# Optimization experiments

Hardware: AMD Instinct MI355X
Metric: run time of the kernel (lower is better)

## Reference

```python
import jax, jax.numpy as jnp
import numpy as np

K = 3  # kernel_size
KK = K * K


def conv2d(x, w, b, stride=1, padding=1, dilation=1):
    out = jax.lax.conv_general_dilated(
        x, w, (stride, stride), [(padding, padding), (padding, padding)],
        rhs_dilation=(dilation, dilation),
        dimension_numbers=('NCHW', 'OIHW', 'NCHW'))
    return out + b[None, :, None, None]


def bilinear_gather(x, py, px):
    # x: [B,C,H,W]; py,px: [B,KK,H,W] float sampling coords (zero outside).
    B, C, H, W = x.shape
    y0 = jnp.floor(py)
    x0 = jnp.floor(px)
    wy1 = py - y0
    wx1 = px - x0
    xf = x.reshape(B, C, H * W)

    def corner(yc, xc, wgt):
        valid = (yc >= 0) & (yc <= H - 1) & (xc >= 0) & (xc <= W - 1)
        yi = jnp.clip(yc, 0, H - 1).astype(jnp.int32)
        xi = jnp.clip(xc, 0, W - 1).astype(jnp.int32)
        idx = (yi * W + xi).reshape(B, 1, -1)  # [B,1,KK*H*W]
        v = jnp.take_along_axis(xf, jnp.broadcast_to(idx, (B, C, idx.shape[-1])), axis=2)
        v = v.reshape(B, C, *yc.shape[1:])  # [B,C,KK,H,W]
        return v * (wgt * valid)[:, None]

    return (corner(y0, x0, (1 - wy1) * (1 - wx1)) +
            corner(y0, x0 + 1, (1 - wy1) * wx1) +
            corner(y0 + 1, x0, wy1 * (1 - wx1)) +
            corner(y0 + 1, x0 + 1, wy1 * wx1))


def modulated_deform_conv(x, offset, mask, w, b, stride=1, padding=1, dilation=1):
    B, C, H, W = x.shape
    Ho, Wo = offset.shape[2], offset.shape[3]
    off = offset.reshape(B, KK, 2, Ho, Wo)
    dy, dx = off[:, :, 0], off[:, :, 1]  # [B,KK,Ho,Wo]
    ki, kj = jnp.meshgrid(jnp.arange(K), jnp.arange(K), indexing='ij')
    ki = ki.reshape(-1).astype(x.dtype)  # [KK]
    kj = kj.reshape(-1).astype(x.dtype)
    base_y = (jnp.arange(Ho) * stride - padding).astype(x.dtype)
    base_x = (jnp.arange(Wo) * stride - padding).astype(x.dtype)
    py = base_y[None, None, :, None] + (ki * dilation)[None, :, None, None] + dy
    px = base_x[None, None, None, :] + (kj * dilation)[None, :, None, None] + dx
    x_off = bilinear_gather(x, py, px)              # [B,C,KK,Ho,Wo]
    x_off = x_off * mask[:, None]                   # modulation
    w_flat = w.reshape(w.shape[0], C, KK)           # [O,C,KK]
    out = jnp.einsum('bckhw,ock->bohw', x_off, w_flat)
    return out + b[None, :, None, None]


def setup_inputs() -> dict:
    key = jax.random.key(0)
    ks = jax.random.split(key, 7)
    B, C, O, H, W = 8, 64, 64, 128, 128
    x = jax.random.normal(ks[0], (B, C, H, W), dtype=jnp.float32)
    # offset/mask predictor convs (zero-init in the module; randomized small here
    # so offsets/masks are non-trivial for kernel correctness testing)
    p_w = jax.random.normal(ks[1], (2 * KK, C, 3, 3), dtype=jnp.float32) * 0.02
    p_b = jax.random.normal(ks[2], (2 * KK,), dtype=jnp.float32) * 0.1
    m_w = jax.random.normal(ks[3], (KK, C, 3, 3), dtype=jnp.float32) * 0.02
    m_b = jax.random.normal(ks[4], (KK,), dtype=jnp.float32) * 0.1
    # deformable conv weights
    d_w = jax.random.normal(ks[5], (O, C, K, K), dtype=jnp.float32) * (1.0 / np.sqrt(C * KK))
    d_b = jax.random.normal(ks[6], (O,), dtype=jnp.float32) * 0.01
    return {"x": x, "p_w": p_w, "p_b": p_b, "m_w": m_w, "m_b": m_b, "d_w": d_w, "d_b": d_b}


def reference(x, p_w, p_b, m_w, m_b, d_w, d_b):
    offset = conv2d(x, p_w, p_b, stride=1, padding=1, dilation=1)   # [B,18,H,W]
    mask = jax.nn.sigmoid(conv2d(x, m_w, m_b, stride=1, padding=1, dilation=1))  # [B,9,H,W]
    out = modulated_deform_conv(x, offset, mask, d_w, d_b, stride=1, padding=1, dilation=1)
    return (out, offset)
```

## Files before the change

### kernel.cpp

```cpp
#include <hip/hip_runtime.h>
#include <math.h>

#define KK 9
#define BB 8
#define CC 64
#define OO 64
#define HH 128
#define WW 128
#define HWSZ (HH*WW)

typedef _Float16 half8 __attribute__((ext_vector_type(8)));
typedef float    floatx4 __attribute__((ext_vector_type(4)));

#define WP_ELEMS (9*2*4*32*8)
#define WD_ELEMS (9*2*4*64*8)
#define XH_ELEMS ((size_t)BB*HWSZ*64)
#define NCONV 2048

__global__ __launch_bounds__(256) void prep(
    const float* __restrict__ x,
    const float* __restrict__ p_w, const float* __restrict__ m_w,
    const float* __restrict__ d_w,
    _Float16* __restrict__ Wp, _Float16* __restrict__ Wd, _Float16* __restrict__ x_h,
    int conv_blocks)
{
    const int blk = blockIdx.x;
    const int tid = threadIdx.x;
    if (blk < conv_blocks) {
        __shared__ _Float16 sh[64][72];
        const int b    = blk >> 8;
        const int pix0 = (blk & 255) * 64;
        const float* xb = x + (size_t)b*CC*HWSZ + pix0;
        {
            const int p     = tid & 63;
            const int cbase = tid >> 6;
            #pragma unroll
            for (int j = 0; j < 16; ++j) {
                const int c = j*4 + cbase;
                sh[p][c] = (_Float16)xb[(size_t)c*HWSZ + p];
            }
        }
        __syncthreads();
        {
            const int p  = tid >> 2;
            const int c0 = (tid & 3) * 16;
            _Float16* dst = x_h + ((size_t)b*HWSZ + pix0 + p)*64 + c0;
            *(half8*)dst       = *(const half8*)&sh[p][c0];
            *(half8*)(dst + 8) = *(const half8*)&sh[p][c0 + 8];
        }
    } else {
        const int i = (blk - conv_blocks)*256 + tid;
        if (i < WP_ELEMS) {
            const int e = i & 7, n = (i>>3)&31, quad = (i>>8)&3, ks = (i>>10)&1, k = i>>11;
            const int c = ks*32 + quad*8 + e;
            float v = 0.f;
            if (n < 18)      v = p_w[(n*CC + c)*KK + k];
            else if (n < 27) v = m_w[((n-18)*CC + c)*KK + k];
            Wp[i] = (_Float16)v;
        } else if (i < WP_ELEMS + WD_ELEMS) {
            const int j = i - WP_ELEMS;
            const int e = j & 7, o = (j>>3)&63, quad = (j>>9)&3, ks = (j>>11)&1, k = j>>12;
            const int c = ks*32 + quad*8 + e;
            Wd[j] = (_Float16)d_w[(o*CC + c)*KK + k];
        }
    }
}

__global__ __launch_bounds__(256, 3) void dcn_fused(
    const _Float16* __restrict__ x_h,
    const _Float16* __restrict__ Wp, const _Float16* __restrict__ Wd,
    const float* __restrict__ p_b, const float* __restrict__ m_b,
    const float* __restrict__ db,
    float* __restrict__ out, float* __restrict__ offset_out)
{
    __shared__ alignas(16) float    T[27*68];
    __shared__ alignas(16) _Float16 WS[2][4096];

    const int tid  = threadIdx.x;
    const int wv   = tid >> 6;
    const int lane = tid & 63;
    const int quad = lane >> 4;
    const int l15  = lane & 15;
    const int b    = blockIdx.x & 7;
    const int seg  = blockIdx.x >> 3;
    const int row  = seg >> 1;
    const int col0 = (seg & 1) * 64;
    const int pix0 = row * WW + col0;
    const int px   = wv*16 + l15;
    const int wx   = col0 + px;
    const _Float16* xbh = x_h + (size_t)b*HWSZ*64;

    half8 ws0a = *(const half8*)(Wd + tid*16);
    half8 ws0b = *(const half8*)(Wd + tid*16 + 8);

    floatx4 accp[2];
    accp[0] = (floatx4)0.f; accp[1] = (floatx4)0.f;
    #pragma unroll
    for (int k = 0; k < 9; ++k) {
        const int hy = row + k/3 - 1;
        const int hx = wx  + k%3 - 1;
        const bool vld = (hy >= 0) & (hy < HH) & (hx >= 0) & (hx < WW);
        const _Float16* ap = xbh + (size_t)(vld ? hy*WW + hx : 0)*64 + quad*8;
        const half8 z = (half8)(_Float16)0.f;
        half8 a0 = *(const half8*)ap;
        half8 a1 = *(const half8*)(ap + 32);
        a0 = vld ? a0 : z;
        a1 = vld ? a1 : z;
        const _Float16* wp = Wp + k*2048 + quad*256 + l15*8;
        #pragma unroll
        for (int ks = 0; ks < 2; ++ks) {
            const half8 af = ks ? a1 : a0;
            accp[0] = __builtin_amdgcn_mfma_f32_16x16x32_f16(af, *(const half8*)(wp + ks*1024),       accp[0], 0, 0, 0);
            accp[1] = __builtin_amdgcn_mfma_f32_16x16x32_f16(af, *(const half8*)(wp + ks*1024 + 128), accp[1], 0, 0, 0);
        }
    }

    #pragma unroll
    for (int nt = 0; nt < 2; ++nt) {
        const int ch = nt*16 + l15;
        if (ch < 27) {
            const float bias = (ch < 18) ? p_b[ch] : m_b[ch-18];
            #pragma unroll
            for (int r = 0; r < 4; ++r)
                T[ch*68 + wv*16 + quad*4 + r] = accp[nt][r] + bias;
        }
    }
    {
        _Float16* wd = &WS[0][tid*16];
        *(half8*)wd     = ws0a;
        *(half8*)(wd+8) = ws0b;
    }
    __syncthreads();

    {
        float* offp = offset_out + (size_t)b*18*HWSZ + pix0;
        #pragma unroll
        for (int j = 0; j < 5; ++j) {
            const int idx = j*256 + tid;
            if (idx < 18*64) {
                const int ch = idx >> 6, p2i = idx & 63;
                offp[ch*HWSZ + p2i] = T[ch*68 + p2i];
            }
        }
    }

    const int p2   = wv*16 + (lane >> 2);
    const int part = lane & 3;
    const int wx2  = col0 + p2;
    const int bidx = ((l15 << 2) | quad) << 2;

    float dyk[9], dxk[9], mkk[9];
    #pragma unroll
    for (int k = 0; k < 9; ++k) {
        dyk[k] = T[(2*k  )*68 + p2];
        dxk[k] = T[(2*k+1)*68 + p2];
        mkk[k] = 1.f / (1.f + expf(-T[(18+k)*68 + p2]));
    }

    floatx4 acc[4];
    #pragma unroll
    for (int nt = 0; nt < 4; ++nt) acc[nt] = (floatx4)0.f;

    #pragma unroll
    for (int k = 0; k < 9; ++k) {
        half8 wsa, wsb;
        if (k < 8) {
            const _Float16* wsrc = Wd + (k+1)*4096 + tid*16;
            wsa = *(const half8*)wsrc;
            wsb = *(const half8*)(wsrc + 8);
        }

        const float dy = dyk[k], dx = dxk[k], mk = mkk[k];
        const float py  = (float)(row - 1 + k/3) + dy;
        const float pxf = (float)(wx2 - 1 + k%3) + dx;
        const float y0f = floorf(py), x0f = floorf(pxf);
        const int   iy0 = (int)y0f,   ix0 = (int)x0f;
        const float wy1 = py - y0f,   wx1 = pxf - x0f;
        const float wy0 = 1.f - wy1,  wx0 = 1.f - wx1;
        const bool vy0 = ((unsigned)iy0     < (unsigned)HH);
        const bool vy1 = ((unsigned)(iy0+1) < (unsigned)HH);
        const bool vx0 = ((unsigned)ix0     < (unsigned)WW);
        const bool vx1 = ((unsigned)(ix0+1) < (unsigned)WW);
        const int cy0 = min(max(iy0,   0), HH-1), cy1 = min(max(iy0+1, 0), HH-1);
        const int cx0 = min(max(ix0,   0), WW-1), cx1 = min(max(ix0+1, 0), WW-1);
        const int i0 = cy0*WW+cx0, i1 = cy0*WW+cx1, i2 = cy1*WW+cx0, i3 = cy1*WW+cx1;
        const _Float16 g0 = (_Float16)(wy0*wx0*((vy0&vx0) ? mk : 0.f));
        const _Float16 g1 = (_Float16)(wy0*wx1*((vy0&vx1) ? mk : 0.f));
        const _Float16 g2 = (_Float16)(wy1*wx0*((vy1&vx0) ? mk : 0.f));
        const _Float16 g3 = (_Float16)(wy1*wx1*((vy1&vx1) ? mk : 0.f));

        const _Float16* c0p = xbh + (size_t)i0*64 + part*8;
        const _Float16* c1p = xbh + (size_t)i1*64 + part*8;
        const _Float16* c2p = xbh + (size_t)i2*64 + part*8;
        const _Float16* c3p = xbh + (size_t)i3*64 + part*8;
        const half8 p0l = *(const half8*)c0p, p0h = *(const half8*)(c0p + 32);
        const half8 p1l = *(const half8*)c1p, p1h = *(const half8*)(c1p + 32);
        const half8 p2l = *(const half8*)c2p, p2h = *(const half8*)(c2p + 32);
        const half8 p3l = *(const half8*)c3p, p3h = *(const half8*)(c3p + 32);
        const half8 lo = p0l*g0 + p1l*g1 + p2l*g2 + p3l*g3;
        const half8 hi = p0h*g0 + p1h*g1 + p2h*g2 + p3h*g3;

        union U { half8 h; int i[4]; };
        U ulo, uhi, a0u, a1u;
        ulo.h = lo; uhi.h = hi;
        #pragma unroll
        for (int d = 0; d < 4; ++d) {
            a0u.i[d] = __builtin_amdgcn_ds_bpermute(bidx, ulo.i[d]);
            a1u.i[d] = __builtin_amdgcn_ds_bpermute(bidx, uhi.i[d]);
        }

        #pragma unroll
        for (int ks = 0; ks < 2; ++ks) {
            const half8 af = ks ? a1u.h : a0u.h;
            const _Float16* wsp = &WS[k&1][ks*2048 + quad*512 + l15*8];
            #pragma unroll
            for (int nt = 0; nt < 4; ++nt)
                acc[nt] = __builtin_amdgcn_mfma_f32_16x16x32_f16(af, *(const half8*)(wsp + nt*128), acc[nt], 0, 0, 0);
        }

        if (k < 8) {
            _Float16* wd = &WS[(k+1)&1][tid*16];
            *(half8*)wd     = wsa;
            *(half8*)(wd+8) = wsb;
        }
        __syncthreads();
    }

    float* T2 = (float*)&WS[0][0];
    #pragma unroll
    for (int oc = 0; oc < 4; ++oc) {
        #pragma unroll
        for (int r = 0; r < 4; ++r)
            T2[l15*68 + wv*16 + quad*4 + r] = acc[oc][r];
        __syncthreads();
        #pragma unroll
        for (int j = 0; j < 4; ++j) {
            const int idx = j*256 + tid;
            const int o16 = idx >> 6, pp = idx & 63;
            out[((size_t)b*OO + oc*16 + o16)*HWSZ + pix0 + pp] = T2[o16*68 + pp] + db[oc*16 + o16];
        }
        __syncthreads();
    }
}

__global__ __launch_bounds__(256, 4) void dcn_fused_lds(
    const float* __restrict__ x,
    const _Float16* __restrict__ Wp, const _Float16* __restrict__ Wd,
    const float* __restrict__ p_b, const float* __restrict__ m_b,
    const float* __restrict__ db,
    float* __restrict__ out, float* __restrict__ offset_out)
{
    __shared__ alignas(16) _Float16 A_sh[128][72];
    __shared__ alignas(16) _Float16 WM_sh[32*72];
    __shared__ alignas(16) _Float16 Wd_sh[64][72];

    const int tid   = threadIdx.x;
    const int wv    = tid >> 6;
    const int lane  = tid & 63;
    const int quad  = lane >> 4;
    const int l15   = lane & 15;
    const int b     = blockIdx.x & 7;
    const int row   = blockIdx.x >> 3;
    const int pix0  = row * WW;
    const int p     = tid & 127;
    const int chalf = (tid >> 7) * 32;
    const int h = row, w = p;
    const float* xb = x + (size_t)b*CC*HWSZ;
    _Float16 (*W_sh)[72] = (_Float16 (*)[72])WM_sh;

    floatx4 accp[2][2];
    #pragma unroll
    for (int mt = 0; mt < 2; ++mt)
        #pragma unroll
        for (int nt = 0; nt < 2; ++nt) accp[mt][nt] = (floatx4)0.f;

    for (int k = 0; k < 9; ++k) {
        {
            const int n  = tid >> 3;
            const int c0 = (tid & 7) * 8;
            *(half8*)&W_sh[n][c0] =
                *(const half8*)(Wp + k*2048 + (c0>>5)*1024 + ((c0>>3)&3)*256 + n*8);
        }
        const int hy = h + (k/3) - 1;
        const int wx = w + (k%3) - 1;
        const bool vld = (hy >= 0) & (hy < HH) & (wx >= 0) & (wx < WW);
        const float* xs = xb + hy*WW + wx;
        #pragma unroll
        for (int cb = 0; cb < 4; ++cb) {
            union { half8 v; _Float16 e[8]; } u;
            #pragma unroll
            for (int j = 0; j < 8; ++j)
                u.e[j] = (_Float16)(vld ? xs[(size_t)(chalf + cb*8 + j)*HWSZ] : 0.f);
            *(half8*)&A_sh[p][chalf + cb*8] = u.v;
        }
        __syncthreads();
        #pragma unroll
        for (int ks = 0; ks < 2; ++ks) {
            half8 bf[2];
            #pragma unroll
            for (int nt = 0; nt < 2; ++nt)
                bf[nt] = *(const half8*)&W_sh[nt*16 + l15][ks*32 + quad*8];
            #pragma unroll
            for (int mt = 0; mt < 2; ++mt) {
                half8 af = *(const half8*)&A_sh[wv*32 + mt*16 + l15][ks*32 + quad*8];
                accp[mt][0] = __builtin_amdgcn_mfma_f32_16x16x32_f16(af, bf[0], accp[mt][0], 0, 0, 0);
                accp[mt][1] = __builtin_amdgcn_mfma_f32_16x16x32_f16(af, bf[1], accp[mt][1], 0, 0, 0);
            }
        }
        __syncthreads();
    }

    float (*T)[132] = (float (*)[132])&A_sh[0][0];
    #pragma unroll
    for (int nt = 0; nt < 2; ++nt) {
        const int ch = nt*16 + l15;
        if (ch < 27) {
            #pragma unroll
            for (int mt = 0; mt < 2; ++mt)
                #pragma unroll
                for (int r = 0; r < 4; ++r)
                    T[ch][wv*32 + mt*16 + quad*4 + r] = accp[mt][nt][r];
        }
    }
    __syncthreads();

    float dyk[9], dxk[9], mkk[9];
    float* offp = offset_out + (size_t)b*18*HWSZ + pix0;
    #pragma unroll
    for (int k = 0; k < 9; ++k) {
        dyk[k] = T[2*k][p]   + p_b[2*k];
        dxk[k] = T[2*k+1][p] + p_b[2*k+1];
        mkk[k] = 1.f / (1.f + expf(-(T[18+k][p] + m_b[k])));
    }
    if (tid < 128) {
        #pragma unroll
        for (int k = 0; k < 9; ++k) {
            offp[(2*k  )*HWSZ + p] = dyk[k];
            offp[(2*k+1)*HWSZ + p] = dxk[k];
        }
    }
    __syncthreads();

    floatx4 acc[2][4];
    #pragma unroll
    for (int mt = 0; mt < 2; ++mt)
        #pragma unroll
        for (int nt = 0; nt < 4; ++nt) acc[mt][nt] = (floatx4)0.f;

    for (int k = 0; k < 9; ++k) {
        {
            const int o  = tid >> 2;
            const int c0 = (tid & 3) * 16;
            *(half8*)&Wd_sh[o][c0] =
                *(const half8*)(Wd + k*4096 + (c0>>5)*2048 + ((c0>>3)&3)*512 + o*8);
            const int c8 = c0 + 8;
            *(half8*)&Wd_sh[o][c8] =
                *(const half8*)(Wd + k*4096 + (c8>>5)*2048 + ((c8>>3)&3)*512 + o*8);
        }
        const float mk = mkk[k];
        const float py = (float)(h - 1 + k/3) + dyk[k];
        const float px = (float)(w - 1 + k%3) + dxk[k];
        const float y0f = floorf(py), x0f = floorf(px);
        const int   iy0 = (int)y0f,   ix0 = (int)x0f;
        const float wy1 = py - y0f,   wx1 = px - x0f;
        const float wy0 = 1.f - wy1,  wx0 = 1.f - wx1;
        const bool vy0 = (iy0   >= 0) & (iy0   < HH);
        const bool vy1 = (iy0+1 >= 0) & (iy0+1 < HH);
        const bool vx0 = (ix0   >= 0) & (ix0   < WW);
        const bool vx1 = (ix0+1 >= 0) & (ix0+1 < WW);
        const int cy0 = min(max(iy0,   0), HH-1), cy1 = min(max(iy0+1, 0), HH-1);
        const int cx0 = min(max(ix0,   0), WW-1), cx1 = min(max(ix0+1, 0), WW-1);
        const int i0 = cy0*WW+cx0; const float w0 = wy0*wx0*((vy0&vx0) ? mk : 0.f);
        const int i1 = cy0*WW+cx1; const float w1 = wy0*wx1*((vy0&vx1) ? mk : 0.f);
        const int i2 = cy1*WW+cx0; const float w2 = wy1*wx0*((vy1&vx0) ? mk : 0.f);
        const int i3 = cy1*WW+cx1; const float w3 = wy1*wx1*((vy1&vx1) ? mk : 0.f);
        #pragma unroll
        for (int cb = 0; cb < 4; ++cb) {
            union { half8 v; _Float16 e[8]; } u;
            #pragma unroll
            for (int j = 0; j < 8; ++j) {
                const float* xc = xb + (size_t)(chalf + cb*8 + j)*HWSZ;
                u.e[j] = (_Float16)(w0*xc[i0] + w1*xc[i1] + w2*xc[i2] + w3*xc[i3]);
            }
            *(half8*)&A_sh[p][chalf + cb*8] = u.v;
        }
        __syncthreads();
        #pragma unroll
        for (int ks = 0; ks < 2; ++ks) {
            half8 bf[4];
            #pragma unroll
            for (int nt = 0; nt < 4; ++nt)
                bf[nt] = *(const half8*)&Wd_sh[nt*16 + l15][ks*32 + quad*8];
            #pragma unroll
            for (int mt = 0; mt < 2; ++mt) {
                half8 af = *(const half8*)&A_sh[wv*32 + mt*16 + l15][ks*32 + quad*8];
                #pragma unroll
                for (int nt = 0; nt < 4; ++nt)
                    acc[mt][nt] = __builtin_amdgcn_mfma_f32_16x16x32_f16(af, bf[nt], acc[mt][nt], 0, 0, 0);
            }
        }
        __syncthreads();
    }

    float (*T2)[132] = (float (*)[132])&A_sh[0][0];
    #pragma unroll
    for (int oc = 0; oc < 4; ++oc) {
        #pragma unroll
        for (int mt = 0; mt < 2; ++mt)
            #pragma unroll
            for (int r = 0; r < 4; ++r)
                T2[l15][wv*32 + mt*16 + quad*4 + r] = acc[mt][oc][r];
        __syncthreads();
        #pragma unroll
        for (int j = 0; j < 8; ++j) {
            const int idx = tid + j*256;
            const int o16 = idx >> 7, pp = idx & 127;
            out[((size_t)b*OO + oc*16 + o16)*HWSZ + pix0 + pp] = T2[o16][pp] + db[oc*16 + o16];
        }
        __syncthreads();
    }
}

extern "C" void kernel_launch(void* const* d_in, const int* in_sizes, int n_in,
                              void* d_out, int out_size, void* d_ws, size_t ws_size,
                              hipStream_t stream) {
    const float* x   = (const float*)d_in[0];
    const float* p_w = (const float*)d_in[1];
    const float* p_b = (const float*)d_in[2];
    const float* m_w = (const float*)d_in[3];
    const float* m_b = (const float*)d_in[4];
    const float* dw  = (const float*)d_in[5];
    const float* db  = (const float*)d_in[6];

    float* out        = (float*)d_out;
    float* offset_out = out + (size_t)BB*OO*HWSZ;

    _Float16* Wp  = (_Float16*)d_ws;
    _Float16* Wd  = Wp + WP_ELEMS;
    _Float16* x_h = Wd + WD_ELEMS;

    const int nrep = (WP_ELEMS + WD_ELEMS + 255) / 256;
    const size_t need = (size_t)(WP_ELEMS + WD_ELEMS + XH_ELEMS) * sizeof(_Float16);
    if (ws_size >= need) {
        prep<<<dim3(NCONV + nrep), 256, 0, stream>>>(x, p_w, m_w, dw, Wp, Wd, x_h, NCONV);
        dcn_fused<<<dim3(256*BB), 256, 0, stream>>>(x_h, Wp, Wd, p_b, m_b, db, out, offset_out);
    } else {
        prep<<<dim3(nrep), 256, 0, stream>>>(x, p_w, m_w, dw, Wp, Wd, x_h, 0);
        dcn_fused_lds<<<dim3(128*BB), 256, 0, stream>>>(x, Wp, Wd, p_b, m_b, db, out, offset_out);
    }
}
```

Measured before the change: 150.0 us.

## Drop LDS weight staging, read deform weights from global, raise occupancy

```diff
diff --git a/kernel.cpp b/kernel.cpp
--- a/kernel.cpp
+++ b/kernel.cpp
@@ -66,15 +66,14 @@
     }
 }
 
-__global__ __launch_bounds__(256, 3) void dcn_fused(
+__global__ __launch_bounds__(256, 6) void dcn_fused(
     const _Float16* __restrict__ x_h,
     const _Float16* __restrict__ Wp, const _Float16* __restrict__ Wd,
     const float* __restrict__ p_b, const float* __restrict__ m_b,
     const float* __restrict__ db,
     float* __restrict__ out, float* __restrict__ offset_out)
 {
-    __shared__ alignas(16) float    T[27*68];
-    __shared__ alignas(16) _Float16 WS[2][4096];
+    __shared__ alignas(16) float T[27*68];
 
     const int tid  = threadIdx.x;
     const int wv   = tid >> 6;
@@ -86,33 +85,40 @@
     const int row  = seg >> 1;
     const int col0 = (seg & 1) * 64;
     const int pix0 = row * WW + col0;
-    const int px   = wv*16 + l15;
-    const int wx   = col0 + px;
     const _Float16* xbh = x_h + (size_t)b*HWSZ*64;
 
-    half8 ws0a = *(const half8*)(Wd + tid*16);
-    half8 ws0b = *(const half8*)(Wd + tid*16 + 8);
+    const int p2   = wv*16 + (lane >> 2);
+    const int part = lane & 3;
+    const int wx2  = col0 + p2;
+    const int bidx = ((l15 << 2) | quad) << 2;
+
+    union U { half8 h; int i[4]; };
 
     floatx4 accp[2];
     accp[0] = (floatx4)0.f; accp[1] = (floatx4)0.f;
     #pragma unroll
     for (int k = 0; k < 9; ++k) {
         const int hy = row + k/3 - 1;
-        const int hx = wx  + k%3 - 1;
+        const int hx = wx2 + k%3 - 1;
         const bool vld = (hy >= 0) & (hy < HH) & (hx >= 0) & (hx < WW);
-        const _Float16* ap = xbh + (size_t)(vld ? hy*WW + hx : 0)*64 + quad*8;
+        const _Float16* ap = xbh + (size_t)(vld ? hy*WW + hx : 0)*64 + part*8;
         const half8 z = (half8)(_Float16)0.f;
         half8 a0 = *(const half8*)ap;
         half8 a1 = *(const half8*)(ap + 32);
         a0 = vld ? a0 : z;
         a1 = vld ? a1 : z;
+        U u0, u1, b0, b1;
+        u0.h = a0; u1.h = a1;
+        #pragma unroll
+        for (int d = 0; d < 4; ++d) {
+            b0.i[d] = __builtin_amdgcn_ds_bpermute(bidx, u0.i[d]);
+            b1.i[d] = __builtin_amdgcn_ds_bpermute(bidx, u1.i[d]);
+        }
         const _Float16* wp = Wp + k*2048 + quad*256 + l15*8;
-        #pragma unroll
-        for (int ks = 0; ks < 2; ++ks) {
-            const half8 af = ks ? a1 : a0;
-            accp[0] = __builtin_amdgcn_mfma_f32_16x16x32_f16(af, *(const half8*)(wp + ks*1024),       accp[0], 0, 0, 0);
-            accp[1] = __builtin_amdgcn_mfma_f32_16x16x32_f16(af, *(const half8*)(wp + ks*1024 + 128), accp[1], 0, 0, 0);
-        }
+        accp[0] = __builtin_amdgcn_mfma_f32_16x16x32_f16(b0.h, *(const half8*)(wp),              accp[0], 0, 0, 0);
+        accp[1] = __builtin_amdgcn_mfma_f32_16x16x32_f16(b0.h, *(const half8*)(wp + 128),        accp[1], 0, 0, 0);
+        accp[0] = __builtin_amdgcn_mfma_f32_16x16x32_f16(b1.h, *(const half8*)(wp + 1024),       accp[0], 0, 0, 0);
+        accp[1] = __builtin_amdgcn_mfma_f32_16x16x32_f16(b1.h, *(const half8*)(wp + 1024 + 128), accp[1], 0, 0, 0);
     }
 
     #pragma unroll
@@ -125,11 +131,6 @@
                 T[ch*68 + wv*16 + quad*4 + r] = accp[nt][r] + bias;
         }
     }
-    {
-        _Float16* wd = &WS[0][tid*16];
-        *(half8*)wd     = ws0a;
-        *(half8*)(wd+8) = ws0b;
-    }
     __syncthreads();
 
     {
@@ -138,17 +139,11 @@
         for (int j = 0; j < 5; ++j) {
             const int idx = j*256 + tid;
             if (idx < 18*64) {
-                const int ch = idx >> 6, p2i = idx & 63;
-                offp[ch*HWSZ + p2i] = T[ch*68 + p2i];
+                const int ch = idx >> 6, pp = idx & 63;
+                offp[ch*HWSZ + pp] = T[ch*68 + pp];
             }
         }
     }
-
-    const int p2   = wv*16 + (lane >> 2);
-    const int part = lane & 3;
-    const int wx2  = col0 + p2;
-    const int bidx = ((l15 << 2) | quad) << 2;
-
     float dyk[9], dxk[9], mkk[9];
     #pragma unroll
     for (int k = 0; k < 9; ++k) {
@@ -163,13 +158,6 @@
 
     #pragma unroll
     for (int k = 0; k < 9; ++k) {
-        half8 wsa, wsb;
-        if (k < 8) {
-            const _Float16* wsrc = Wd + (k+1)*4096 + tid*16;
-            wsa = *(const half8*)wsrc;
-            wsb = *(const half8*)(wsrc + 8);
-        }
-
         const float dy = dyk[k], dx = dxk[k], mk = mkk[k];
         const float py  = (float)(row - 1 + k/3) + dy;
         const float pxf = (float)(wx2 - 1 + k%3) + dx;
@@ -200,7 +188,6 @@
         const half8 lo = p0l*g0 + p1l*g1 + p2l*g2 + p3l*g3;
         const half8 hi = p0h*g0 + p1h*g1 + p2h*g2 + p3h*g3;
 
-        union U { half8 h; int i[4]; };
         U ulo, uhi, a0u, a1u;
         ulo.h = lo; uhi.h = hi;
         #pragma unroll
@@ -212,21 +199,15 @@
         #pragma unroll
         for (int ks = 0; ks < 2; ++ks) {
             const half8 af = ks ? a1u.h : a0u.h;
-            const _Float16* wsp = &WS[k&1][ks*2048 + quad*512 + l15*8];
+            const _Float16* wdp = Wd + k*4096 + ks*2048 + quad*512 + l15*8;
             #pragma unroll
             for (int nt = 0; nt < 4; ++nt)
-                acc[nt] = __builtin_amdgcn_mfma_f32_16x16x32_f16(af, *(const half8*)(wsp + nt*128), acc[nt], 0, 0, 0);
-        }
-
-        if (k < 8) {
-            _Float16* wd = &WS[(k+1)&1][tid*16];
-            *(half8*)wd     = wsa;
-            *(half8*)(wd+8) = wsb;
-        }
-        __syncthreads();
-    }
-
-    float* T2 = (float*)&WS[0][0];
+                acc[nt] = __builtin_amdgcn_mfma_f32_16x16x32_f16(af, *(const half8*)(wdp + nt*128), acc[nt], 0, 0, 0);
+        }
+    }
+
+    __syncthreads();
+    float* T2 = T;
     #pragma unroll
     for (int oc = 0; oc < 4; ++oc) {
         #pragma unroll
```

After: 159.7 us. +6.5%, slower.
